# Optimization experiments

Hardware: AMD Instinct MI355X
Metric: run time of the kernel (lower is better)

The kernel has to match this reference:

```python
import jax, jax.numpy as jnp
import numpy as np


def setup_inputs() -> dict:
    key = jax.random.key(0)
    k1, k2 = jax.random.split(key)
    B, L, K, C = 8, 4096, 32, 64
    x = jax.random.normal(k1, (B, L, K, C), dtype=jnp.float32)
    mask = jax.random.randint(k2, (B, L, K, C), 0, 2, dtype=jnp.int32)
    return {"x": x, "mask": mask}


def reference(x, mask):
    # Masked mean over the sequence dim (axis=1), broadcast back to [B, L, K, C].
    # Equivalent to torch.mean(x[b, mask[b,:,k,c].bool(), k, c]) per (b,k,c),
    # with empty-mask NaNs replaced by 0.
    m = mask.astype(x.dtype)
    s = jnp.sum(x * m, axis=1)          # [B, K, C]
    cnt = jnp.sum(m, axis=1)            # [B, K, C]
    mean = jnp.where(cnt > 0, s / jnp.maximum(cnt, 1), jnp.zeros_like(s))
    return jnp.broadcast_to(mean[:, None, :, :], x.shape)
```

## Files before the change

kernel.cpp:

```cpp
#include <hip/hip_runtime.h>

#define B_DIM 8
#define L_DIM 4096
#define KC 2048
#define LCB  16
#define PT   512

__global__ __launch_bounds__(PT) void partial_k(const float* __restrict__ x,
                                                const int* __restrict__ mask,
                                                float* __restrict__ psum,
                                                float* __restrict__ pcnt,
                                                int nseg, int lrows) {
    const int b   = blockIdx.x / nseg;
    const int seg = blockIdx.x % nseg;
    const int t   = threadIdx.x;

    const long base = ((long)b * L_DIM + (long)seg * lrows) * KC + t * 4;

    float4 s = make_float4(0.f, 0.f, 0.f, 0.f);
    float4 c = make_float4(0.f, 0.f, 0.f, 0.f);

    #pragma unroll 4
    for (int l = 0; l < lrows; ++l) {
        const float4 xv = *(const float4*)(x    + base + (long)l * KC);
        const int4   mv = *(const int4*)  (mask + base + (long)l * KC);
        float m0 = (float)mv.x, m1 = (float)mv.y, m2 = (float)mv.z, m3 = (float)mv.w;
        s.x = fmaf(xv.x, m0, s.x);  c.x += m0;
        s.y = fmaf(xv.y, m1, s.y);  c.y += m1;
        s.z = fmaf(xv.z, m2, s.z);  c.z += m2;
        s.w = fmaf(xv.w, m3, s.w);  c.w += m3;
    }

    const long po = ((long)b * nseg + seg) * KC + t * 4;
    *(float4*)(&psum[po]) = s;
    *(float4*)(&pcnt[po]) = c;
}

__global__ __launch_bounds__(256) void mean_k(const float* __restrict__ psum,
                                              const float* __restrict__ pcnt,
                                              float* __restrict__ mean,
                                              int nseg) {
    const int i = blockIdx.x * 256 + threadIdx.x;
    const int b = i / KC;
    const int j = i % KC;

    float s = 0.f, c = 0.f;
    #pragma unroll 4
    for (int seg = 0; seg < nseg; ++seg) {
        const long o = ((long)b * nseg + seg) * KC + j;
        s += psum[o];
        c += pcnt[o];
    }
    mean[i] = (c > 0.f) ? (s / c) : 0.f;
}

__global__ __launch_bounds__(PT) void bcast_k(const float* __restrict__ mean,
                                              float* __restrict__ out) {
    const int blocks_per_b = L_DIM / LCB;
    const int b    = blockIdx.x / blocks_per_b;
    const int lseg = blockIdx.x % blocks_per_b;
    const int t    = threadIdx.x;

    const float4 v = *(const float4*)(&mean[(long)b * KC + t * 4]);

    const long base = ((long)b * L_DIM + (long)lseg * LCB) * KC + t * 4;
    #pragma unroll
    for (int l = 0; l < LCB; ++l)
        *(float4*)(out + base + (long)l * KC) = v;
}

extern "C" void kernel_launch(void* const* d_in, const int* in_sizes, int n_in,
                              void* d_out, int out_size, void* d_ws, size_t ws_size,
                              hipStream_t stream) {
    const float* x    = (const float*)d_in[0];
    const int*   mask = (const int*)d_in[1];
    float*       out  = (float*)d_out;
    float*       ws   = (float*)d_ws;

    int nseg = 128;
    while (nseg > 1 &&
           (size_t)(2ul * B_DIM * nseg * KC + B_DIM * KC) * 4ul > ws_size)
        nseg >>= 1;
    const int lrows = L_DIM / nseg;

    float* psum = ws;
    float* pcnt = ws + (long)B_DIM * nseg * KC;
    float* mean = ws + 2l * B_DIM * nseg * KC;

    partial_k<<<B_DIM * nseg, PT, 0, stream>>>(x, mask, psum, pcnt,
                                               nseg, lrows);

    mean_k<<<(B_DIM * KC) / 256, 256, 0, stream>>>(psum, pcnt, mean, nseg);

    bcast_k<<<B_DIM * (L_DIM / LCB), PT, 0, stream>>>(mean, out);
}
```

Before: 196.2 us.

## Software-pipeline partial reduction with inline-asm prefetch ring and more segments

The partial-sum kernel now issues eight rows of x and mask loads ahead through inline global_load_dwordx4, using explicit vmcnt waits and scheduling barriers so sixteen loads stay in flight while earlier rows are consumed. The segment count doubles, to 256, so each block handles fewer rows and more blocks are launched. The aim is to hide memory latency in the bandwidth-bound reduction pass. The risks are higher register pressure from the sixteen 128-bit buffers, and the hand-written waitcnt logic assumes that lrows is a multiple of 8 and at least 8.

```diff
diff --git a/kernel.cpp b/kernel.cpp
--- a/kernel.cpp
+++ b/kernel.cpp
@@ -5,6 +5,29 @@
 #define KC 2048
 #define LCB  16
 #define PT   512
+
+typedef float f4 __attribute__((ext_vector_type(4)));
+typedef int   i4 __attribute__((ext_vector_type(4)));
+
+#define GLD_F4(dst, p) asm volatile("global_load_dwordx4 %0, %1, off" : "=v"(dst) : "v"(p))
+#define GLD_I4(dst, p) asm volatile("global_load_dwordx4 %0, %1, off" : "=v"(dst) : "v"(p))
+#define WAITV(n) asm volatile("s_waitcnt vmcnt(" #n ")" ::: "memory")
+#define SB() __builtin_amdgcn_sched_barrier(0)
+
+#define CONS(J) do {                                        \
+    float m0 = (float)mv##J[0], m1 = (float)mv##J[1];       \
+    float m2 = (float)mv##J[2], m3 = (float)mv##J[3];       \
+    s[0] = fmaf(xv##J[0], m0, s[0]);  c[0] += m0;           \
+    s[1] = fmaf(xv##J[1], m1, s[1]);  c[1] += m1;           \
+    s[2] = fmaf(xv##J[2], m2, s[2]);  c[2] += m2;           \
+    s[3] = fmaf(xv##J[3], m3, s[3]);  c[3] += m3;           \
+} while (0)
+
+#define STEP(J, XN, MN) do {                                \
+    WAITV(14); SB(); CONS(J);                               \
+    GLD_F4(xv##J, (XN) + (long)(J) * KC);                   \
+    GLD_I4(mv##J, (MN) + (long)(J) * KC);                   \
+} while (0)
 
 __global__ __launch_bounds__(PT) void partial_k(const float* __restrict__ x,
                                                 const int* __restrict__ mask,
@@ -16,24 +39,49 @@
     const int t   = threadIdx.x;
 
     const long base = ((long)b * L_DIM + (long)seg * lrows) * KC + t * 4;
+    const float* xp = x + base;
+    const int*   mp = mask + base;
 
-    float4 s = make_float4(0.f, 0.f, 0.f, 0.f);
-    float4 c = make_float4(0.f, 0.f, 0.f, 0.f);
+    f4 s = {0.f, 0.f, 0.f, 0.f};
+    f4 c = {0.f, 0.f, 0.f, 0.f};
 
-    #pragma unroll 4
-    for (int l = 0; l < lrows; ++l) {
-        const float4 xv = *(const float4*)(x    + base + (long)l * KC);
-        const int4   mv = *(const int4*)  (mask + base + (long)l * KC);
-        float m0 = (float)mv.x, m1 = (float)mv.y, m2 = (float)mv.z, m3 = (float)mv.w;
-        s.x = fmaf(xv.x, m0, s.x);  c.x += m0;
-        s.y = fmaf(xv.y, m1, s.y);  c.y += m1;
-        s.z = fmaf(xv.z, m2, s.z);  c.z += m2;
-        s.w = fmaf(xv.w, m3, s.w);  c.w += m3;
+    f4 xv0, xv1, xv2, xv3, xv4, xv5, xv6, xv7;
+    i4 mv0, mv1, mv2, mv3, mv4, mv5, mv6, mv7;
+
+    GLD_F4(xv0, xp + 0l * KC);  GLD_I4(mv0, mp + 0l * KC);
+    GLD_F4(xv1, xp + 1l * KC);  GLD_I4(mv1, mp + 1l * KC);
+    GLD_F4(xv2, xp + 2l * KC);  GLD_I4(mv2, mp + 2l * KC);
+    GLD_F4(xv3, xp + 3l * KC);  GLD_I4(mv3, mp + 3l * KC);
+    GLD_F4(xv4, xp + 4l * KC);  GLD_I4(mv4, mp + 4l * KC);
+    GLD_F4(xv5, xp + 5l * KC);  GLD_I4(mv5, mp + 5l * KC);
+    GLD_F4(xv6, xp + 6l * KC);  GLD_I4(mv6, mp + 6l * KC);
+    GLD_F4(xv7, xp + 7l * KC);  GLD_I4(mv7, mp + 7l * KC);
+
+    for (int l0 = 0; l0 < lrows - 8; l0 += 8) {
+        const float* xn = xp + (long)(l0 + 8) * KC;
+        const int*   mn = mp + (long)(l0 + 8) * KC;
+        STEP(0, xn, mn);
+        STEP(1, xn, mn);
+        STEP(2, xn, mn);
+        STEP(3, xn, mn);
+        STEP(4, xn, mn);
+        STEP(5, xn, mn);
+        STEP(6, xn, mn);
+        STEP(7, xn, mn);
     }
 
+    WAITV(14); SB(); CONS(0);
+    WAITV(12); SB(); CONS(1);
+    WAITV(10); SB(); CONS(2);
+    WAITV(8);  SB(); CONS(3);
+    WAITV(6);  SB(); CONS(4);
+    WAITV(4);  SB(); CONS(5);
+    WAITV(2);  SB(); CONS(6);
+    WAITV(0);  SB(); CONS(7);
+
     const long po = ((long)b * nseg + seg) * KC + t * 4;
-    *(float4*)(&psum[po]) = s;
-    *(float4*)(&pcnt[po]) = c;
+    *(f4*)(&psum[po]) = s;
+    *(f4*)(&pcnt[po]) = c;
 }
 
 __global__ __launch_bounds__(256) void mean_k(const float* __restrict__ psum,
@@ -77,8 +125,8 @@
     float*       out  = (float*)d_out;
     float*       ws   = (float*)d_ws;
 
-    int nseg = 128;
-    while (nseg > 1 &&
+    int nseg = 256;
+    while (nseg > 8 &&
            (size_t)(2ul * B_DIM * nseg * KC + B_DIM * KC) * 4ul > ws_size)
         nseg >>= 1;
     const int lrows = L_DIM / nseg;
```

New measurement: 217.3 us. +10.8%, slower.
